# Optimization experiments

Hardware: AMD Instinct MI355X
Metric: run time of the kernel (lower is better)

## Reference

```python
import jax, jax.numpy as jnp
import numpy as np
from jax import lax

DIM = 64
HEADS = 4
GN_EPS = 1e-5
L2_EPS = 1e-12


def conv2d(x, w, b=None, pad=0, groups=1, dil=1):
    out = lax.conv_general_dilated(
        x, w, window_strides=(1, 1), padding=[(pad, pad), (pad, pad)],
        rhs_dilation=(dil, dil), dimension_numbers=('NCHW', 'OIHW', 'NCHW'),
        feature_group_count=groups)
    if b is not None:
        out = out + b[None, :, None, None]
    return out


def group_norm2(x, gamma, beta):
    # GroupNorm with 2 groups over (C/2, H, W)
    b, c, h, w = x.shape
    xr = x.reshape(b, 2, c // 2, h, w)
    mu = xr.mean(axis=(2, 3, 4), keepdims=True)
    var = xr.var(axis=(2, 3, 4), keepdims=True)
    xn = ((xr - mu) * lax.rsqrt(var + GN_EPS)).reshape(b, c, h, w)
    return xn * gamma[None, :, None, None] + beta[None, :, None, None]


def lka(x, c0w, c0b, csw, csb, c1w, c1b, gn_g, gn_b):
    dim = c0w.shape[0]
    a = conv2d(x, c0w, c0b, pad=2, groups=dim)           # depthwise 5x5
    a = conv2d(a, csw, csb, pad=3, groups=dim, dil=3)    # depthwise 3x3, dilation 3
    a = conv2d(a, c1w, c1b, pad=0)                       # 1x1 pointwise
    return jax.nn.leaky_relu(group_norm2(a, gn_g, gn_b), 0.2)


def l2norm_lastdim(t):
    n = jnp.sqrt(jnp.sum(t * t, axis=-1, keepdims=True))
    return t / jnp.maximum(n, L2_EPS)


def setup_inputs() -> dict:
    key = jax.random.key(0)
    ks = jax.random.split(key, 24)
    B, C, H, W = 4, DIM, 256, 256
    s = 0.05

    def rn(k, shape, scale=s):
        return jax.random.normal(k, shape, dtype=jnp.float32) * scale

    d2 = 2 * DIM
    inp = {
        'x': jax.random.normal(ks[0], (B, C, H, W), dtype=jnp.float32),
        'y': jax.random.normal(ks[1], (B, C, H, W), dtype=jnp.float32),
        # 1x1 projections (bias=False)
        'kv_w': rn(ks[2], (d2, DIM, 1, 1)),
        'q_w': rn(ks[3], (DIM, DIM, 1, 1)),
        'proj_w': rn(ks[4], (DIM, DIM, 1, 1)),
        # kv LKA (C_hid = C_out = 128)
        'kv_c0_w': rn(ks[5], (d2, 1, 5, 5)), 'kv_c0_b': rn(ks[6], (d2,)),
        'kv_cs_w': rn(ks[7], (d2, 1, 3, 3)), 'kv_cs_b': rn(ks[8], (d2,)),
        'kv_c1_w': rn(ks[9], (d2, d2, 1, 1)), 'kv_c1_b': rn(ks[10], (d2,)),
        'kv_gn_g': jnp.ones((d2,), jnp.float32), 'kv_gn_b': jnp.zeros((d2,), jnp.float32),
        # q LKA (C_hid = C_out = 64)
        'q_c0_w': rn(ks[11], (DIM, 1, 5, 5)), 'q_c0_b': rn(ks[12], (DIM,)),
        'q_cs_w': rn(ks[13], (DIM, 1, 3, 3)), 'q_cs_b': rn(ks[14], (DIM,)),
        'q_c1_w': rn(ks[15], (DIM, DIM, 1, 1)), 'q_c1_b': rn(ks[16], (DIM,)),
        'q_gn_g': jnp.ones((DIM,), jnp.float32), 'q_gn_b': jnp.zeros((DIM,), jnp.float32),
        'temperature': jnp.ones((HEADS, 1, 1), jnp.float32),
    }
    return inp


def reference(x, y, kv_w, q_w, proj_w,
              kv_c0_w, kv_c0_b, kv_cs_w, kv_cs_b, kv_c1_w, kv_c1_b, kv_gn_g, kv_gn_b,
              q_c0_w, q_c0_b, q_cs_w, q_cs_b, q_c1_w, q_c1_b, q_gn_g, q_gn_b,
              temperature):
    b, c, h, w = x.shape
    kv = lka(conv2d(y, kv_w), kv_c0_w, kv_c0_b, kv_cs_w, kv_cs_b, kv_c1_w, kv_c1_b, kv_gn_g, kv_gn_b)
    k, v = jnp.split(kv, 2, axis=1)
    q = lka(conv2d(x, q_w), q_c0_w, q_c0_b, q_cs_w, q_cs_b, q_c1_w, q_c1_b, q_gn_g, q_gn_b)

    ch = c // HEADS
    hw = h * w
    q = q.reshape(b, HEADS, ch, hw)
    k = k.reshape(b, HEADS, ch, hw)
    v = v.reshape(b, HEADS, ch, hw)

    q = l2norm_lastdim(q)
    k = l2norm_lastdim(k)

    attn = jnp.einsum('bhcn,bhdn->bhcd', q, k) * temperature[None]  # [b,H,ch,ch]
    attn = jax.nn.softmax(attn, axis=-1)
    out = jnp.einsum('bhcd,bhdn->bhcn', attn, v).reshape(b, c, h, w)
    return conv2d(out, proj_w)
```

## Files before the change

### kernel.cpp

```cpp
#include <hip/hip_runtime.h>

#define HW 65536
#define IMG 256

__device__ __forceinline__ float hsum4(float4 v) { return v.x + v.y + v.z + v.w; }
__device__ __forceinline__ float lrelu(float v) { return v >= 0.f ? v : 0.2f * v; }

template<int CIT, bool GNIN>
__global__ __launch_bounds__(256, 4)
void conv1x1_v3(const float* __restrict__ in, int in_cs,
                const float* __restrict__ w, int w_bstride,
                const float* __restrict__ bias,
                float* __restrict__ out, int out_cs, int out_coff,
                float* __restrict__ stats, int gsel,
                const float* __restrict__ gstats,
                const float* __restrict__ g_gamma, const float* __restrict__ g_beta,
                int g_coff, float g_Nf)
{
    const int b  = blockIdx.y;
    const int j  = threadIdx.x & 63;
    const int wv = __builtin_amdgcn_readfirstlane((int)(threadIdx.x >> 6));
    const int co0 = wv * 16;
    const int q0 = blockIdx.x * 64;
    const float4* in4 = (const float4*)in + (size_t)b * in_cs * (HW/4) + q0 + j;
    const float* wb = w + (size_t)b * w_bstride;

    float gmean = 0.f, grstd = 0.f;
    if (GNIN) {
        gmean = gstats[b*4] / g_Nf;
        float var = gstats[b*4 + 1] / g_Nf - gmean * gmean;
        grstd = rsqrtf(var + 1e-5f);
    }

    float4 acc[16];
    #pragma unroll
    for (int k = 0; k < 16; ++k) {
        float bv = bias ? bias[co0 + k] : 0.f;
        acc[k] = make_float4(bv, bv, bv, bv);
    }

    #pragma unroll 4
    for (int ci = 0; ci < CIT; ++ci) {
        float4 x = in4[(size_t)ci * (HW/4)];
        if (GNIN) {
            float A = g_gamma[g_coff + ci] * grstd;
            float B = g_beta[g_coff + ci] - gmean * A;
            x.x = lrelu(fmaf(x.x, A, B));
            x.y = lrelu(fmaf(x.y, A, B));
            x.z = lrelu(fmaf(x.z, A, B));
            x.w = lrelu(fmaf(x.w, A, B));
        }
        const float* wr = wb + ci;
        #pragma unroll
        for (int k = 0; k < 16; ++k) {
            float wk = wr[(size_t)(co0 + k) * CIT];
            acc[k].x = fmaf(wk, x.x, acc[k].x);
            acc[k].y = fmaf(wk, x.y, acc[k].y);
            acc[k].z = fmaf(wk, x.z, acc[k].z);
            acc[k].w = fmaf(wk, x.w, acc[k].w);
        }
    }

    if (!GNIN && stats) {
        float s = 0.f, ss = 0.f;
        #pragma unroll
        for (int k = 0; k < 16; ++k) {
            s  += acc[k].x + acc[k].y + acc[k].z + acc[k].w;
            ss += acc[k].x*acc[k].x + acc[k].y*acc[k].y
                + acc[k].z*acc[k].z + acc[k].w*acc[k].w;
        }
        #pragma unroll
        for (int o = 32; o; o >>= 1) { s += __shfl_down(s, o, 64); ss += __shfl_down(ss, o, 64); }
        if (j == 0) {
            const int g = (gsel < 0) ? (co0 >= 32 ? 1 : 0) : 0;
            float* st = stats + (size_t)b*4 + g*2;
            atomicAdd(st,     s);
            atomicAdd(st + 1, ss);
        }
    }

    __syncthreads();

    float4* out4 = (float4*)out + ((size_t)b * out_cs + out_coff) * (HW/4) + q0 + j;
    #pragma unroll
    for (int k = 0; k < 16; ++k)
        out4[(size_t)(co0 + k) * (HW/4)] = acc[k];
}

template<int TAPS, int DIL>
__global__ __launch_bounds__(256)
void dwconv_v2(const float* __restrict__ in, int in_cs, int in_coff,
               const float* __restrict__ wt, const float* __restrict__ bias, int w_coff,
               float* __restrict__ out, int out_cs, int out_coff)
{
    constexpr int HALO = DIL * (TAPS/2);
    constexpr int TW = 64, TH = 16;
    constexpr int LW = TW + 2*HALO;
    constexpr int LH = TH + 2*HALO;
    constexpr int RS = (LW + 3) & ~3;
    __shared__ float Xs[LH * RS];
    const int z = blockIdx.z;
    const int c = z & 63, b = z >> 6;
    const int x0 = blockIdx.x * TW, y0 = blockIdx.y * TH;
    const float* ip = in + ((size_t)b*in_cs + in_coff + c) * HW;
    const int cw = w_coff + c;
    float wk[TAPS*TAPS];
    #pragma unroll
    for (int i = 0; i < TAPS*TAPS; ++i) wk[i] = wt[cw*TAPS*TAPS + i];
    const float bv = bias[cw];
    for (int idx = threadIdx.x; idx < LH*LW; idx += 256) {
        int ly = idx / LW, lx = idx - ly*LW;
        int gy = y0 + ly - HALO, gx = x0 + lx - HALO;
        float v = 0.f;
        if (gy >= 0 && gy < IMG && gx >= 0 && gx < IMG)
            v = ip[gy*IMG + gx];
        Xs[ly*RS + lx] = v;
    }
    __syncthreads();
    const int qx = (threadIdx.x & 15) * 4;
    const int ly = threadIdx.x >> 4;
    float o0 = bv, o1 = bv, o2 = bv, o3 = bv;
    #pragma unroll
    for (int ky = 0; ky < TAPS; ++ky) {
        const float* row = &Xs[(ly + ky*DIL)*RS + qx];
        float win[(TAPS-1)*DIL + 4];
        #pragma unroll
        for (int i = 0; i < (TAPS-1)*DIL + 4; ++i) win[i] = row[i];
        #pragma unroll
        for (int kx = 0; kx < TAPS; ++kx) {
            float wv_ = wk[ky*TAPS + kx];
            o0 = fmaf(wv_, win[kx*DIL + 0], o0);
            o1 = fmaf(wv_, win[kx*DIL + 1], o1);
            o2 = fmaf(wv_, win[kx*DIL + 2], o2);
            o3 = fmaf(wv_, win[kx*DIL + 3], o3);
        }
    }
    *(float4*)(out + ((size_t)b*out_cs + out_coff + c) * HW + (size_t)(y0 + ly)*IMG + x0 + qx) =
        make_float4(o0, o1, o2, o3);
}

__global__ __launch_bounds__(256)
void attn_dot_v3(const float* __restrict__ q, const float* __restrict__ k,
                 const float* __restrict__ stQ, const float* __restrict__ stK,
                 const float* __restrict__ qg, const float* __restrict__ qb,
                 const float* __restrict__ kg, const float* __restrict__ kb,
                 float* __restrict__ attn_raw,
                 float* __restrict__ ssq, float* __restrict__ ssk)
{
    __shared__ float4 qs[2048], ks[2048];
    __shared__ float sred[512];
    const int h = blockIdx.y, b = blockIdx.z;
    const int t0 = blockIdx.x * 128;
    const int cc = threadIdx.x & 15;
    const int ch = h*16 + cc;

    const int gq = (ch >= 32) ? 1 : 0;
    float mq = stQ[b*4 + gq*2] / (32.f * HW);
    float vq = stQ[b*4 + gq*2 + 1] / (32.f * HW) - mq*mq;
    const float Aq = qg[ch] * rsqrtf(vq + 1e-5f);
    const float Bq = qb[ch] - mq * Aq;
    float mk = stK[b*4] / (64.f * HW);
    float vk = stK[b*4 + 1] / (64.f * HW) - mk*mk;
    const float Ak = kg[ch] * rsqrtf(vk + 1e-5f);
    const float Bk = kb[ch] - mk * Ak;

    const float4* q4 = (const float4*)q + ((size_t)b*64 + ch) * (HW/4) + t0;
    const float4* k4 = (const float4*)k + ((size_t)b*64 + ch) * (HW/4) + t0;
    float sq_acc = 0.f, sk_acc = 0.f;
    #pragma unroll
    for (int s = 0; s < 8; ++s) {
        int t = (threadIdx.x >> 4) + s*16;
        float4 v = q4[t];
        v.x = lrelu(fmaf(v.x, Aq, Bq)); v.y = lrelu(fmaf(v.y, Aq, Bq));
        v.z = lrelu(fmaf(v.z, Aq, Bq)); v.w = lrelu(fmaf(v.w, Aq, Bq));
        sq_acc += v.x*v.x + v.y*v.y + v.z*v.z + v.w*v.w;
        qs[t*16 + cc] = v;
        float4 u = k4[t];
        u.x = lrelu(fmaf(u.x, Ak, Bk)); u.y = lrelu(fmaf(u.y, Ak, Bk));
        u.z = lrelu(fmaf(u.z, Ak, Bk)); u.w = lrelu(fmaf(u.w, Ak, Bk));
        sk_acc += u.x*u.x + u.y*u.y + u.z*u.z + u.w*u.w;
        ks[t*16 + cc] = u;
    }
    sred[threadIdx.x]       = sq_acc;
    sred[256 + threadIdx.x] = sk_acc;
    __syncthreads();

    const int p   = threadIdx.x & 63;
    const int sub = threadIdx.x >> 6;
    const int c0 = (p >> 3) << 1, d0 = (p & 7) << 1;
    float4 a00 = make_float4(0,0,0,0), a01 = a00, a10 = a00, a11 = a00;
    #pragma unroll
    for (int i = 0; i < 32; ++i) {
        int t = sub*32 + i;
        float4 qa = qs[t*16 + c0], qb_ = qs[t*16 + c0 + 1];
        float4 ka = ks[t*16 + d0], kb_ = ks[t*16 + d0 + 1];
        a00.x = fmaf(qa.x, ka.x, a00.x); a00.y = fmaf(qa.y, ka.y, a00.y);
        a00.z = fmaf(qa.z, ka.z, a00.z); a00.w = fmaf(qa.w, ka.w, a00.w);
        a01.x = fmaf(qa.x, kb_.x, a01.x); a01.y = fmaf(qa.y, kb_.y, a01.y);
        a01.z = fmaf(qa.z, kb_.z, a01.z); a01.w = fmaf(qa.w, kb_.w, a01.w);
        a10.x = fmaf(qb_.x, ka.x, a10.x); a10.y = fmaf(qb_.y, ka.y, a10.y);
        a10.z = fmaf(qb_.z, ka.z, a10.z); a10.w = fmaf(qb_.w, ka.w, a10.w);
        a11.x = fmaf(qb_.x, kb_.x, a11.x); a11.y = fmaf(qb_.y, kb_.y, a11.y);
        a11.z = fmaf(qb_.z, kb_.z, a11.z); a11.w = fmaf(qb_.w, kb_.w, a11.w);
    }
    float* ar = attn_raw + ((size_t)b*4 + h) * 256;
    atomicAdd(&ar[(c0  )*16 + d0  ], hsum4(a00));
    atomicAdd(&ar[(c0  )*16 + d0+1], hsum4(a01));
    atomicAdd(&ar[(c0+1)*16 + d0  ], hsum4(a10));
    atomicAdd(&ar[(c0+1)*16 + d0+1], hsum4(a11));

    if (threadIdx.x < 16) {
        float s = 0.f;
        #pragma unroll
        for (int jj = 0; jj < 16; ++jj) s += sred[threadIdx.x + 16*jj];
        atomicAdd(&ssq[b*64 + h*16 + threadIdx.x], s);
    } else if (threadIdx.x < 32) {
        const int c2 = threadIdx.x - 16;
        float s = 0.f;
        #pragma unroll
        for (int jj = 0; jj < 16; ++jj) s += sred[256 + c2 + 16*jj];
        atomicAdd(&ssk[b*64 + h*16 + c2], s);
    }
}

__global__ __launch_bounds__(256)
void attn_softmax_v2(const float* __restrict__ attn_raw,
                     const float* __restrict__ ssq, const float* __restrict__ ssk,
                     const float* __restrict__ temp, float* __restrict__ attn)
{
    const int h = blockIdx.x, b = blockIdx.y;
    const int c = threadIdx.x >> 4, d = threadIdx.x & 15;
    const float nq = fmaxf(sqrtf(ssq[b*64 + h*16 + c]), 1e-12f);
    const float nk = fmaxf(sqrtf(ssk[b*64 + h*16 + d]), 1e-12f);
    float logit = attn_raw[((size_t)b*4 + h)*256 + c*16 + d] / (nq * nk) * temp[h];
    float m = logit;
    #pragma unroll
    for (int o = 8; o; o >>= 1) m = fmaxf(m, __shfl_xor(m, o, 16));
    float e = expf(logit - m);
    float s = e;
    #pragma unroll
    for (int o = 8; o; o >>= 1) s += __shfl_xor(s, o, 16);
    attn[((size_t)b*4 + h)*256 + c*16 + d] = e / s;
}

__global__ __launch_bounds__(256)
void build_m_v2(const float* __restrict__ attn, const float* __restrict__ proj_w,
                float* __restrict__ M)
{
    const int b = blockIdx.x;
    for (int i = threadIdx.x; i < 4096; i += 256) {
        int co = i >> 6, ci = i & 63;
        int h = ci >> 4, d = ci & 15;
        float s = 0.f;
        #pragma unroll
        for (int cc = 0; cc < 16; ++cc)
            s += proj_w[co*64 + h*16 + cc] * attn[((size_t)b*4 + h)*256 + cc*16 + d];
        M[(size_t)b*4096 + i] = s;
    }
}

extern "C" void kernel_launch(void* const* d_in, const int* in_sizes, int n_in,
                              void* d_out, int out_size, void* d_ws, size_t ws_size,
                              hipStream_t stream)
{
    const float* x       = (const float*)d_in[0];
    const float* y       = (const float*)d_in[1];
    const float* kv_w    = (const float*)d_in[2];
    const float* q_w     = (const float*)d_in[3];
    const float* proj_w  = (const float*)d_in[4];
    const float* kv_c0_w = (const float*)d_in[5];
    const float* kv_c0_b = (const float*)d_in[6];
    const float* kv_cs_w = (const float*)d_in[7];
    const float* kv_cs_b = (const float*)d_in[8];
    const float* kv_c1_w = (const float*)d_in[9];
    const float* kv_c1_b = (const float*)d_in[10];
    const float* kv_gn_g = (const float*)d_in[11];
    const float* kv_gn_b = (const float*)d_in[12];
    const float* q_c0_w  = (const float*)d_in[13];
    const float* q_c0_b  = (const float*)d_in[14];
    const float* q_cs_w  = (const float*)d_in[15];
    const float* q_cs_b  = (const float*)d_in[16];
    const float* q_c1_w  = (const float*)d_in[17];
    const float* q_c1_b  = (const float*)d_in[18];
    const float* q_gn_g  = (const float*)d_in[19];
    const float* q_gn_b  = (const float*)d_in[20];
    const float* temp    = (const float*)d_in[21];

    float* ws       = (float*)d_ws;
    float* statsKV  = ws;
    float* statsQ   = ws + 16;
    float* sumsq_k  = ws + 32;
    float* sumsq_q  = ws + 288;
    float* attn_raw = ws + 544;
    float* attn     = ws + 4640;
    float* Mw       = ws + 8736;
    float* big      = (float*)((char*)d_ws + 131072);

    const size_t perb_bytes = (size_t)192 * HW * 4;
    int nb = 1;
    if      (ws_size >= 131072 + 4*perb_bytes) nb = 4;
    else if (ws_size >= 131072 + 2*perb_bytes) nb = 2;

    hipMemsetAsync(d_ws, 0, 102400, stream);
    dim3 blk(256);

    for (int b0 = 0; b0 < 4; b0 += nb) {
        const float* xb = x + (size_t)b0*64*HW;
        const float* yb = y + (size_t)b0*64*HW;
        float* H1 = big;
        float* H2 = big + (size_t)nb*128*HW;
        float* O  = (float*)d_out + (size_t)b0*64*HW;
        float* Q1 = H1;
        float* Q2 = H1 + (size_t)nb*64*HW;
        float* stK = statsKV + b0*4;
        float* stQ = statsQ  + b0*4;
        float* ssk = sumsq_k + b0*64;
        float* ssq = sumsq_q + b0*64;
        float* arw = attn_raw + b0*1024;
        float* atn = attn     + b0*1024;
        float* Mb  = Mw       + b0*4096;

        dim3 gconv(256, nb);
        dim3 gdw(4, 16, nb*64);

        conv1x1_v3<64,false><<<gconv, blk, 0, stream>>>(yb, 64, kv_w,       0, nullptr, H1, 128, 0,
                                                        nullptr, 0, nullptr, nullptr, nullptr, 0, 0.f);
        conv1x1_v3<64,false><<<gconv, blk, 0, stream>>>(yb, 64, kv_w+64*64, 0, nullptr, H1, 128, 64,
                                                        nullptr, 0, nullptr, nullptr, nullptr, 0, 0.f);
        dwconv_v2<5,1><<<gdw, blk, 0, stream>>>(H1, 128, 0,  kv_c0_w, kv_c0_b, 0,  H2, 64, 0);
        dwconv_v2<5,1><<<gdw, blk, 0, stream>>>(H1, 128, 64, kv_c0_w, kv_c0_b, 64, O,  64, 0);
        dwconv_v2<3,3><<<gdw, blk, 0, stream>>>(H2, 64, 0, kv_cs_w, kv_cs_b, 0,  H1, 128, 0);
        dwconv_v2<3,3><<<gdw, blk, 0, stream>>>(O,  64, 0, kv_cs_w, kv_cs_b, 64, H1, 128, 64);
        conv1x1_v3<128,false><<<gconv, blk, 0, stream>>>(H1, 128, kv_c1_w,        0, kv_c1_b,    H2, 64, 0,
                                                         stK,   0, nullptr, nullptr, nullptr, 0, 0.f);
        conv1x1_v3<128,false><<<gconv, blk, 0, stream>>>(H1, 128, kv_c1_w+64*128, 0, kv_c1_b+64, O,  64, 0,
                                                         stK+2, 0, nullptr, nullptr, nullptr, 0, 0.f);

        conv1x1_v3<64,false><<<gconv, blk, 0, stream>>>(xb, 64, q_w, 0, nullptr, Q1, 64, 0,
                                                        nullptr, 0, nullptr, nullptr, nullptr, 0, 0.f);
        dwconv_v2<5,1><<<gdw, blk, 0, stream>>>(Q1, 64, 0, q_c0_w, q_c0_b, 0, Q2, 64, 0);
        dwconv_v2<3,3><<<gdw, blk, 0, stream>>>(Q2, 64, 0, q_cs_w, q_cs_b, 0, Q1, 64, 0);
        conv1x1_v3<64,false><<<gconv, blk, 0, stream>>>(Q1, 64, q_c1_w, 0, q_c1_b, Q2, 64, 0,
                                                        stQ, -1, nullptr, nullptr, nullptr, 0, 0.f);

        attn_dot_v3<<<dim3(128,4,nb), blk, 0, stream>>>(Q2, H2, stQ, stK,
                                                        q_gn_g, q_gn_b, kv_gn_g, kv_gn_b,
                                                        arw, ssq, ssk);
        attn_softmax_v2<<<dim3(4,nb), blk, 0, stream>>>(arw, ssq, ssk, temp, atn);
        build_m_v2<<<dim3(nb), blk, 0, stream>>>(atn, proj_w, Mb);

        conv1x1_v3<64,true><<<gconv, blk, 0, stream>>>(O, 64, Mw + b0*4096, 4096, nullptr,
                                                       (float*)d_out + (size_t)b0*64*HW, 64, 0,
                                                       nullptr, 0, stK+2, kv_gn_g, kv_gn_b, 64, 64.f*HW);
    }
}
```

Baseline: 1.059 ms.

## Split 1x1 conv output channels across grid z and prefetch input channels

The 1x1 conv kernel now gives each wave 8 output channels instead of 16 and spreads the channel groups across a third grid dimension. This is meant to cut register pressure and raise occupancy (launch bound of 8 blocks). It also adds a 4-deep register prefetch of input channels, fuses the two kv projection launches into one, and drops the barrier on non-GN paths. In exchange, each input pixel column is now read by several blocks instead of one, which adds memory traffic that L2 may or may not absorb.

Measured after the change: 1.439 ms. 35.9% more time.

```diff
diff --git a/kernel.cpp b/kernel.cpp
--- a/kernel.cpp
+++ b/kernel.cpp
@@ -6,9 +6,9 @@
 __device__ __forceinline__ float hsum4(float4 v) { return v.x + v.y + v.z + v.w; }
 __device__ __forceinline__ float lrelu(float v) { return v >= 0.f ? v : 0.2f * v; }
 
-template<int CIT, bool GNIN>
-__global__ __launch_bounds__(256, 4)
-void conv1x1_v3(const float* __restrict__ in, int in_cs,
+template<int CIT, int COPW, bool GNIN>
+__global__ __launch_bounds__(256, (COPW == 8) ? 8 : 4)
+void conv1x1_v4(const float* __restrict__ in, int in_cs,
                 const float* __restrict__ w, int w_bstride,
                 const float* __restrict__ bias,
                 float* __restrict__ out, int out_cs, int out_coff,
@@ -20,7 +20,7 @@
     const int b  = blockIdx.y;
     const int j  = threadIdx.x & 63;
     const int wv = __builtin_amdgcn_readfirstlane((int)(threadIdx.x >> 6));
-    const int co0 = wv * 16;
+    const int co0 = ((int)blockIdx.z * 4 + wv) * COPW;
     const int q0 = blockIdx.x * 64;
     const float4* in4 = (const float4*)in + (size_t)b * in_cs * (HW/4) + q0 + j;
     const float* wb = w + (size_t)b * w_bstride;
@@ -32,16 +32,14 @@
         grstd = rsqrtf(var + 1e-5f);
     }
 
-    float4 acc[16];
-    #pragma unroll
-    for (int k = 0; k < 16; ++k) {
+    float4 acc[COPW];
+    #pragma unroll
+    for (int k = 0; k < COPW; ++k) {
         float bv = bias ? bias[co0 + k] : 0.f;
         acc[k] = make_float4(bv, bv, bv, bv);
     }
 
-    #pragma unroll 4
-    for (int ci = 0; ci < CIT; ++ci) {
-        float4 x = in4[(size_t)ci * (HW/4)];
+    auto fmabody = [&](int ci, float4 x) {
         if (GNIN) {
             float A = g_gamma[g_coff + ci] * grstd;
             float B = g_beta[g_coff + ci] - gmean * A;
@@ -52,19 +50,35 @@
         }
         const float* wr = wb + ci;
         #pragma unroll
-        for (int k = 0; k < 16; ++k) {
+        for (int k = 0; k < COPW; ++k) {
             float wk = wr[(size_t)(co0 + k) * CIT];
             acc[k].x = fmaf(wk, x.x, acc[k].x);
             acc[k].y = fmaf(wk, x.y, acc[k].y);
             acc[k].z = fmaf(wk, x.z, acc[k].z);
             acc[k].w = fmaf(wk, x.w, acc[k].w);
         }
-    }
+    };
+
+    float4 xb[4];
+    #pragma unroll
+    for (int p = 0; p < 4; ++p) xb[p] = in4[(size_t)p * (HW/4)];
+
+    for (int cg = 0; cg < CIT/4 - 1; ++cg) {
+        #pragma unroll
+        for (int u = 0; u < 4; ++u) {
+            const int ci = cg*4 + u;
+            float4 x = xb[u];
+            xb[u] = in4[(size_t)(ci + 4) * (HW/4)];
+            fmabody(ci, x);
+        }
+    }
+    #pragma unroll
+    for (int u = 0; u < 4; ++u) fmabody(CIT - 4 + u, xb[u]);
 
     if (!GNIN && stats) {
         float s = 0.f, ss = 0.f;
         #pragma unroll
-        for (int k = 0; k < 16; ++k) {
+        for (int k = 0; k < COPW; ++k) {
             s  += acc[k].x + acc[k].y + acc[k].z + acc[k].w;
             ss += acc[k].x*acc[k].x + acc[k].y*acc[k].y
                 + acc[k].z*acc[k].z + acc[k].w*acc[k].w;
@@ -79,11 +93,11 @@
         }
     }
 
-    __syncthreads();
+    if (GNIN) __syncthreads();
 
     float4* out4 = (float4*)out + ((size_t)b * out_cs + out_coff) * (HW/4) + q0 + j;
     #pragma unroll
-    for (int k = 0; k < 16; ++k)
+    for (int k = 0; k < COPW; ++k)
         out4[(size_t)(co0 + k) * (HW/4)] = acc[k];
 }
 
@@ -320,27 +334,24 @@
         float* atn = attn     + b0*1024;
         float* Mb  = Mw       + b0*4096;
 
-        dim3 gconv(256, nb);
         dim3 gdw(4, 16, nb*64);
 
-        conv1x1_v3<64,false><<<gconv, blk, 0, stream>>>(yb, 64, kv_w,       0, nullptr, H1, 128, 0,
-                                                        nullptr, 0, nullptr, nullptr, nullptr, 0, 0.f);
-        conv1x1_v3<64,false><<<gconv, blk, 0, stream>>>(yb, 64, kv_w+64*64, 0, nullptr, H1, 128, 64,
+        conv1x1_v4<64,8,false><<<dim3(256,nb,4), blk, 0, stream>>>(yb, 64, kv_w, 0, nullptr, H1, 128, 0,
                                                         nullptr, 0, nullptr, nullptr, nullptr, 0, 0.f);
         dwconv_v2<5,1><<<gdw, blk, 0, stream>>>(H1, 128, 0,  kv_c0_w, kv_c0_b, 0,  H2, 64, 0);
         dwconv_v2<5,1><<<gdw, blk, 0, stream>>>(H1, 128, 64, kv_c0_w, kv_c0_b, 64, O,  64, 0);
         dwconv_v2<3,3><<<gdw, blk, 0, stream>>>(H2, 64, 0, kv_cs_w, kv_cs_b, 0,  H1, 128, 0);
         dwconv_v2<3,3><<<gdw, blk, 0, stream>>>(O,  64, 0, kv_cs_w, kv_cs_b, 64, H1, 128, 64);
-        conv1x1_v3<128,false><<<gconv, blk, 0, stream>>>(H1, 128, kv_c1_w,        0, kv_c1_b,    H2, 64, 0,
+        conv1x1_v4<128,8,false><<<dim3(256,nb,2), blk, 0, stream>>>(H1, 128, kv_c1_w,        0, kv_c1_b,    H2, 64, 0,
                                                          stK,   0, nullptr, nullptr, nullptr, 0, 0.f);
-        conv1x1_v3<128,false><<<gconv, blk, 0, stream>>>(H1, 128, kv_c1_w+64*128, 0, kv_c1_b+64, O,  64, 0,
+        conv1x1_v4<128,8,false><<<dim3(256,nb,2), blk, 0, stream>>>(H1, 128, kv_c1_w+64*128, 0, kv_c1_b+64, O,  64, 0,
                                                          stK+2, 0, nullptr, nullptr, nullptr, 0, 0.f);
 
-        conv1x1_v3<64,false><<<gconv, blk, 0, stream>>>(xb, 64, q_w, 0, nullptr, Q1, 64, 0,
+        conv1x1_v4<64,8,false><<<dim3(256,nb,2), blk, 0, stream>>>(xb, 64, q_w, 0, nullptr, Q1, 64, 0,
                                                         nullptr, 0, nullptr, nullptr, nullptr, 0, 0.f);
         dwconv_v2<5,1><<<gdw, blk, 0, stream>>>(Q1, 64, 0, q_c0_w, q_c0_b, 0, Q2, 64, 0);
         dwconv_v2<3,3><<<gdw, blk, 0, stream>>>(Q2, 64, 0, q_cs_w, q_cs_b, 0, Q1, 64, 0);
-        conv1x1_v3<64,false><<<gconv, blk, 0, stream>>>(Q1, 64, q_c1_w, 0, q_c1_b, Q2, 64, 0,
+        conv1x1_v4<64,8,false><<<dim3(256,nb,2), blk, 0, stream>>>(Q1, 64, q_c1_w, 0, q_c1_b, Q2, 64, 0,
                                                         stQ, -1, nullptr, nullptr, nullptr, 0, 0.f);
 
         attn_dot_v3<<<dim3(128,4,nb), blk, 0, stream>>>(Q2, H2, stQ, stK,
@@ -349,7 +360,7 @@
         attn_softmax_v2<<<dim3(4,nb), blk, 0, stream>>>(arw, ssq, ssk, temp, atn);
         build_m_v2<<<dim3(nb), blk, 0, stream>>>(atn, proj_w, Mb);
 
-        conv1x1_v3<64,true><<<gconv, blk, 0, stream>>>(O, 64, Mw + b0*4096, 4096, nullptr,
+        conv1x1_v4<64,16,true><<<dim3(256,nb,1), blk, 0, stream>>>(O, 64, Mw + b0*4096, 4096, nullptr,
                                                        (float*)d_out + (size_t)b0*64*HW, 64, 0,
                                                        nullptr, 0, stK+2, kv_gn_g, kv_gn_b, 64, 64.f*HW);
     }
```

## Fuse depthwise conv pair in shared memory and merge 1x1 conv launches

Applied to the files above, without the earlier changes.

Replaces the separate depthwise 5x5 and dilated 3x3 kernels with one fused kernel. It computes the 5x5 result, including halo, into shared memory and applies the dilated 3x3 from there, so the intermediate tensor never goes to global memory. The 1x1 convolutions that were split into two 64-channel launches now run as one 512-thread launch covering 128 output channels, and a dual-input variant reads the two halves of the KV hidden tensor directly. Buffers are reassigned to fit this. The cost is recomputing the 5x5 conv over the halo region, more shared memory per block, and larger blocks that may lower occupancy.

Measured after the change: 1.040 ms. About the same (-1.8%).

```diff
diff --git a/kernel.cpp b/kernel.cpp
--- a/kernel.cpp
+++ b/kernel.cpp
@@ -6,9 +6,10 @@
 __device__ __forceinline__ float hsum4(float4 v) { return v.x + v.y + v.z + v.w; }
 __device__ __forceinline__ float lrelu(float v) { return v >= 0.f ? v : 0.2f * v; }
 
-template<int CIT, bool GNIN>
-__global__ __launch_bounds__(256, 4)
-void conv1x1_v3(const float* __restrict__ in, int in_cs,
+template<int CIT, int NW, bool GNIN, bool DUAL>
+__global__ __launch_bounds__(NW*64)
+void conv1x1_v5(const float* __restrict__ in, int in_cs,
+                const float* __restrict__ in2, int in2_cs,
                 const float* __restrict__ w, int w_bstride,
                 const float* __restrict__ bias,
                 float* __restrict__ out, int out_cs, int out_coff,
@@ -22,7 +23,6 @@
     const int wv = __builtin_amdgcn_readfirstlane((int)(threadIdx.x >> 6));
     const int co0 = wv * 16;
     const int q0 = blockIdx.x * 64;
-    const float4* in4 = (const float4*)in + (size_t)b * in_cs * (HW/4) + q0 + j;
     const float* wb = w + (size_t)b * w_bstride;
 
     float gmean = 0.f, grstd = 0.f;
@@ -39,26 +39,38 @@
         acc[k] = make_float4(bv, bv, bv, bv);
     }
 
-    #pragma unroll 4
-    for (int ci = 0; ci < CIT; ++ci) {
-        float4 x = in4[(size_t)ci * (HW/4)];
-        if (GNIN) {
-            float A = g_gamma[g_coff + ci] * grstd;
-            float B = g_beta[g_coff + ci] - gmean * A;
-            x.x = lrelu(fmaf(x.x, A, B));
-            x.y = lrelu(fmaf(x.y, A, B));
-            x.z = lrelu(fmaf(x.z, A, B));
-            x.w = lrelu(fmaf(x.w, A, B));
-        }
-        const float* wr = wb + ci;
-        #pragma unroll
-        for (int k = 0; k < 16; ++k) {
-            float wk = wr[(size_t)(co0 + k) * CIT];
-            acc[k].x = fmaf(wk, x.x, acc[k].x);
-            acc[k].y = fmaf(wk, x.y, acc[k].y);
-            acc[k].z = fmaf(wk, x.z, acc[k].z);
-            acc[k].w = fmaf(wk, x.w, acc[k].w);
-        }
+    const float4* in4a = (const float4*)in + (size_t)b * in_cs * (HW/4) + q0 + j;
+
+    auto run = [&](const float4* base, const float* wrb, int n) {
+        #pragma unroll 4
+        for (int ci = 0; ci < n; ++ci) {
+            float4 x = base[(size_t)ci * (HW/4)];
+            if (GNIN) {
+                float A = g_gamma[g_coff + ci] * grstd;
+                float B = g_beta[g_coff + ci] - gmean * A;
+                x.x = lrelu(fmaf(x.x, A, B));
+                x.y = lrelu(fmaf(x.y, A, B));
+                x.z = lrelu(fmaf(x.z, A, B));
+                x.w = lrelu(fmaf(x.w, A, B));
+            }
+            const float* wr = wrb + ci;
+            #pragma unroll
+            for (int k = 0; k < 16; ++k) {
+                float wk = wr[(size_t)(co0 + k) * CIT];
+                acc[k].x = fmaf(wk, x.x, acc[k].x);
+                acc[k].y = fmaf(wk, x.y, acc[k].y);
+                acc[k].z = fmaf(wk, x.z, acc[k].z);
+                acc[k].w = fmaf(wk, x.w, acc[k].w);
+            }
+        }
+    };
+
+    if (DUAL) {
+        const float4* in4b = (const float4*)in2 + (size_t)b * in2_cs * (HW/4) + q0 + j;
+        run(in4a, wb, 64);
+        run(in4b, wb + 64, 64);
+    } else {
+        run(in4a, wb, CIT);
     }
 
     if (!GNIN && stats) {
@@ -72,75 +84,101 @@
         #pragma unroll
         for (int o = 32; o; o >>= 1) { s += __shfl_down(s, o, 64); ss += __shfl_down(ss, o, 64); }
         if (j == 0) {
-            const int g = (gsel < 0) ? (co0 >= 32 ? 1 : 0) : 0;
+            int g = 0;
+            if (gsel == -1) g = (co0 >= 32) ? 1 : 0;
+            else if (gsel == -2) g = (co0 >= 64) ? 1 : 0;
             float* st = stats + (size_t)b*4 + g*2;
             atomicAdd(st,     s);
             atomicAdd(st + 1, ss);
         }
     }
 
-    __syncthreads();
-
     float4* out4 = (float4*)out + ((size_t)b * out_cs + out_coff) * (HW/4) + q0 + j;
     #pragma unroll
     for (int k = 0; k < 16; ++k)
         out4[(size_t)(co0 + k) * (HW/4)] = acc[k];
 }
 
-template<int TAPS, int DIL>
 __global__ __launch_bounds__(256)
-void dwconv_v2(const float* __restrict__ in, int in_cs, int in_coff,
-               const float* __restrict__ wt, const float* __restrict__ bias, int w_coff,
-               float* __restrict__ out, int out_cs, int out_coff)
-{
-    constexpr int HALO = DIL * (TAPS/2);
-    constexpr int TW = 64, TH = 16;
-    constexpr int LW = TW + 2*HALO;
-    constexpr int LH = TH + 2*HALO;
-    constexpr int RS = (LW + 3) & ~3;
-    __shared__ float Xs[LH * RS];
+void dwfused(const float* __restrict__ in, int in_cs, int in_coff,
+             const float* __restrict__ w5, const float* __restrict__ b5, int w5_coff,
+             const float* __restrict__ w3, const float* __restrict__ b3, int w3_coff,
+             float* __restrict__ out, int out_cs, int out_coff)
+{
+    constexpr int TH = 32, TW = 64;
+    constexpr int IN_H = TH + 10, IN_W = TW + 10;
+    constexpr int MID_H = TH + 6, MID_W = TW + 6;
+    constexpr int IN_RS = IN_W + 2;
+    constexpr int MID_RS = MID_W + 2;
+    __shared__ float Xs[IN_H * IN_RS];
+    __shared__ float Ms[MID_H * MID_RS];
     const int z = blockIdx.z;
     const int c = z & 63, b = z >> 6;
     const int x0 = blockIdx.x * TW, y0 = blockIdx.y * TH;
     const float* ip = in + ((size_t)b*in_cs + in_coff + c) * HW;
-    const int cw = w_coff + c;
-    float wk[TAPS*TAPS];
-    #pragma unroll
-    for (int i = 0; i < TAPS*TAPS; ++i) wk[i] = wt[cw*TAPS*TAPS + i];
-    const float bv = bias[cw];
-    for (int idx = threadIdx.x; idx < LH*LW; idx += 256) {
-        int ly = idx / LW, lx = idx - ly*LW;
-        int gy = y0 + ly - HALO, gx = x0 + lx - HALO;
+
+    float wk5[25];
+    #pragma unroll
+    for (int i = 0; i < 25; ++i) wk5[i] = w5[(size_t)(w5_coff + c)*25 + i];
+    const float bv5 = b5[w5_coff + c];
+    float wk3[9];
+    #pragma unroll
+    for (int i = 0; i < 9; ++i) wk3[i] = w3[(size_t)(w3_coff + c)*9 + i];
+    const float bv3 = b3[w3_coff + c];
+
+    for (int idx = threadIdx.x; idx < IN_H*IN_W; idx += 256) {
+        int ly = idx / IN_W, lx = idx - ly*IN_W;
+        int gy = y0 + ly - 5, gx = x0 + lx - 5;
         float v = 0.f;
         if (gy >= 0 && gy < IMG && gx >= 0 && gx < IMG)
             v = ip[gy*IMG + gx];
-        Xs[ly*RS + lx] = v;
+        Xs[ly*IN_RS + lx] = v;
     }
     __syncthreads();
+
+    for (int idx = threadIdx.x; idx < MID_H*MID_W; idx += 256) {
+        int my = idx / MID_W, mx = idx - my*MID_W;
+        int gy = y0 + my - 3, gx = x0 + mx - 3;
+        float v = 0.f;
+        if (gy >= 0 && gy < IMG && gx >= 0 && gx < IMG) {
+            v = bv5;
+            #pragma unroll
+            for (int ky = 0; ky < 5; ++ky) {
+                const float* xr = &Xs[(my + ky)*IN_RS + mx];
+                #pragma unroll
+                for (int kx = 0; kx < 5; ++kx)
+                    v = fmaf(wk5[ky*5 + kx], xr[kx], v);
+            }
+        }
+        Ms[my*MID_RS + mx] = v;
+    }
+    __syncthreads();
+
     const int qx = (threadIdx.x & 15) * 4;
-    const int ly = threadIdx.x >> 4;
-    float o0 = bv, o1 = bv, o2 = bv, o3 = bv;
-    #pragma unroll
-    for (int ky = 0; ky < TAPS; ++ky) {
-        const float* row = &Xs[(ly + ky*DIL)*RS + qx];
-        float win[(TAPS-1)*DIL + 4];
-        #pragma unroll
-        for (int i = 0; i < (TAPS-1)*DIL + 4; ++i) win[i] = row[i];
-        #pragma unroll
-        for (int kx = 0; kx < TAPS; ++kx) {
-            float wv_ = wk[ky*TAPS + kx];
-            o0 = fmaf(wv_, win[kx*DIL + 0], o0);
-            o1 = fmaf(wv_, win[kx*DIL + 1], o1);
-            o2 = fmaf(wv_, win[kx*DIL + 2], o2);
-            o3 = fmaf(wv_, win[kx*DIL + 3], o3);
-        }
-    }
-    *(float4*)(out + ((size_t)b*out_cs + out_coff + c) * HW + (size_t)(y0 + ly)*IMG + x0 + qx) =
-        make_float4(o0, o1, o2, o3);
+    const int ly0 = threadIdx.x >> 4;
+    float* op = out + ((size_t)b*out_cs + out_coff + c) * HW;
+    #pragma unroll
+    for (int r = 0; r < 2; ++r) {
+        const int oy = ly0 + r*16;
+        float o0 = bv3, o1 = bv3, o2 = bv3, o3 = bv3;
+        #pragma unroll
+        for (int kt = 0; kt < 3; ++kt) {
+            const float* mr = &Ms[(oy + 3*kt)*MID_RS + qx];
+            #pragma unroll
+            for (int kx = 0; kx < 3; ++kx) {
+                float wv_ = wk3[kt*3 + kx];
+                o0 = fmaf(wv_, mr[3*kx + 0], o0);
+                o1 = fmaf(wv_, mr[3*kx + 1], o1);
+                o2 = fmaf(wv_, mr[3*kx + 2], o2);
+                o3 = fmaf(wv_, mr[3*kx + 3], o3);
+            }
+        }
+        *(float4*)(op + (size_t)(y0 + oy)*IMG + x0 + qx) = make_float4(o0, o1, o2, o3);
+    }
 }
 
 __global__ __launch_bounds__(256)
-void attn_dot_v3(const float* __restrict__ q, const float* __restrict__ k,
+void attn_dot_v4(const float* __restrict__ q, const float* __restrict__ k, int k_cs,
                  const float* __restrict__ stQ, const float* __restrict__ stK,
                  const float* __restrict__ qg, const float* __restrict__ qb,
                  const float* __restrict__ kg, const float* __restrict__ kb,
@@ -164,8 +202,8 @@
     const float Ak = kg[ch] * rsqrtf(vk + 1e-5f);
     const float Bk = kb[ch] - mk * Ak;
 
-    const float4* q4 = (const float4*)q + ((size_t)b*64 + ch) * (HW/4) + t0;
-    const float4* k4 = (const float4*)k + ((size_t)b*64 + ch) * (HW/4) + t0;
+    const float4* q4 = (const float4*)q + ((size_t)b*64   + ch) * (HW/4) + t0;
+    const float4* k4 = (const float4*)k + ((size_t)b*k_cs + ch) * (HW/4) + t0;
     float sq_acc = 0.f, sk_acc = 0.f;
     #pragma unroll
     for (int s = 0; s < 8; ++s) {
@@ -310,8 +348,6 @@
         float* H1 = big;
         float* H2 = big + (size_t)nb*128*HW;
         float* O  = (float*)d_out + (size_t)b0*64*HW;
-        float* Q1 = H1;
-        float* Q2 = H1 + (size_t)nb*64*HW;
         float* stK = statsKV + b0*4;
         float* stQ = statsQ  + b0*4;
         float* ssk = sumsq_k + b0*64;
@@ -320,37 +356,35 @@
         float* atn = attn     + b0*1024;
         float* Mb  = Mw       + b0*4096;
 
-        dim3 gconv(256, nb);
-        dim3 gdw(4, 16, nb*64);
-
-        conv1x1_v3<64,false><<<gconv, blk, 0, stream>>>(yb, 64, kv_w,       0, nullptr, H1, 128, 0,
-                                                        nullptr, 0, nullptr, nullptr, nullptr, 0, 0.f);
-        conv1x1_v3<64,false><<<gconv, blk, 0, stream>>>(yb, 64, kv_w+64*64, 0, nullptr, H1, 128, 64,
-                                                        nullptr, 0, nullptr, nullptr, nullptr, 0, 0.f);
-        dwconv_v2<5,1><<<gdw, blk, 0, stream>>>(H1, 128, 0,  kv_c0_w, kv_c0_b, 0,  H2, 64, 0);
-        dwconv_v2<5,1><<<gdw, blk, 0, stream>>>(H1, 128, 64, kv_c0_w, kv_c0_b, 64, O,  64, 0);
-        dwconv_v2<3,3><<<gdw, blk, 0, stream>>>(H2, 64, 0, kv_cs_w, kv_cs_b, 0,  H1, 128, 0);
-        dwconv_v2<3,3><<<gdw, blk, 0, stream>>>(O,  64, 0, kv_cs_w, kv_cs_b, 64, H1, 128, 64);
-        conv1x1_v3<128,false><<<gconv, blk, 0, stream>>>(H1, 128, kv_c1_w,        0, kv_c1_b,    H2, 64, 0,
-                                                         stK,   0, nullptr, nullptr, nullptr, 0, 0.f);
-        conv1x1_v3<128,false><<<gconv, blk, 0, stream>>>(H1, 128, kv_c1_w+64*128, 0, kv_c1_b+64, O,  64, 0,
-                                                         stK+2, 0, nullptr, nullptr, nullptr, 0, 0.f);
-
-        conv1x1_v3<64,false><<<gconv, blk, 0, stream>>>(xb, 64, q_w, 0, nullptr, Q1, 64, 0,
-                                                        nullptr, 0, nullptr, nullptr, nullptr, 0, 0.f);
-        dwconv_v2<5,1><<<gdw, blk, 0, stream>>>(Q1, 64, 0, q_c0_w, q_c0_b, 0, Q2, 64, 0);
-        dwconv_v2<3,3><<<gdw, blk, 0, stream>>>(Q2, 64, 0, q_cs_w, q_cs_b, 0, Q1, 64, 0);
-        conv1x1_v3<64,false><<<gconv, blk, 0, stream>>>(Q1, 64, q_c1_w, 0, q_c1_b, Q2, 64, 0,
-                                                        stQ, -1, nullptr, nullptr, nullptr, 0, 0.f);
-
-        attn_dot_v3<<<dim3(128,4,nb), blk, 0, stream>>>(Q2, H2, stQ, stK,
+        dim3 gdwf(4, 8, nb*64);
+        dim3 gc(256, nb);
+
+        conv1x1_v5<64,8,false,false><<<gc, dim3(512), 0, stream>>>(
+            yb, 64, nullptr, 0, kv_w, 0, nullptr, H1, 128, 0,
+            nullptr, 0, nullptr, nullptr, nullptr, 0, 0.f);
+        dwfused<<<gdwf, blk, 0, stream>>>(H1, 128, 0,  kv_c0_w, kv_c0_b, 0,  kv_cs_w, kv_cs_b, 0,  H2, 64, 0);
+        dwfused<<<gdwf, blk, 0, stream>>>(H1, 128, 64, kv_c0_w, kv_c0_b, 64, kv_cs_w, kv_cs_b, 64, O,  64, 0);
+        conv1x1_v5<128,8,false,true><<<gc, dim3(512), 0, stream>>>(
+            H2, 64, O, 64, kv_c1_w, 0, kv_c1_b, H1, 128, 0,
+            stK, -2, nullptr, nullptr, nullptr, 0, 0.f);
+
+        conv1x1_v5<64,4,false,false><<<gc, blk, 0, stream>>>(
+            xb, 64, nullptr, 0, q_w, 0, nullptr, O, 64, 0,
+            nullptr, 0, nullptr, nullptr, nullptr, 0, 0.f);
+        dwfused<<<gdwf, blk, 0, stream>>>(O, 64, 0, q_c0_w, q_c0_b, 0, q_cs_w, q_cs_b, 0, H2, 64, 0);
+        conv1x1_v5<64,4,false,false><<<gc, blk, 0, stream>>>(
+            H2, 64, nullptr, 0, q_c1_w, 0, q_c1_b, O, 64, 0,
+            stQ, -1, nullptr, nullptr, nullptr, 0, 0.f);
+
+        attn_dot_v4<<<dim3(128,4,nb), blk, 0, stream>>>(O, H1, 128, stQ, stK,
                                                         q_gn_g, q_gn_b, kv_gn_g, kv_gn_b,
                                                         arw, ssq, ssk);
         attn_softmax_v2<<<dim3(4,nb), blk, 0, stream>>>(arw, ssq, ssk, temp, atn);
         build_m_v2<<<dim3(nb), blk, 0, stream>>>(atn, proj_w, Mb);
 
-        conv1x1_v3<64,true><<<gconv, blk, 0, stream>>>(O, 64, Mw + b0*4096, 4096, nullptr,
-                                                       (float*)d_out + (size_t)b0*64*HW, 64, 0,
-                                                       nullptr, 0, stK+2, kv_gn_g, kv_gn_b, 64, 64.f*HW);
-    }
-}
+        conv1x1_v5<64,4,true,false><<<gc, blk, 0, stream>>>(
+            H1 + (size_t)64*HW, 128, nullptr, 0, Mw + b0*4096, 4096, nullptr,
+            (float*)d_out + (size_t)b0*64*HW, 64, 0,
+            nullptr, 0, stK+2, kv_gn_g, kv_gn_b, 64, 64.f*HW);
+    }
+}
```
